# Kernel tuning notes

Measured on AMD Instinct MI355X. Metric: run time of the kernel, lower is better.

The kernel has to match this reference:

```python
import jax, jax.numpy as jnp
import numpy as np

# --- module hyperparameters (from init_kwargs) ---
IN_FEATURES = 256
TAU_MIN = 1.0
TAU_MAX = 20.0
K = 4
ALPHA = 1.0
NTAU = 100
SEQ_LEN = 2048
N_S = NTAU + 2 * K  # 108 taustars including k padding on both sides


def _laplace_constants():
    # c = (tau_max/tau_min)**(1/(ntau-1)) - 1
    c = (TAU_MAX / TAU_MIN) ** (1.0 / (NTAU - 1)) - 1.0
    tau_star = TAU_MIN * (1.0 + c) ** jnp.arange(-K, NTAU + K, dtype=jnp.float32)  # (N_S,)
    s = K / tau_star                      # (N_S,) decay rates
    e_s = jnp.exp(-s)                     # (N_S,)
    return s, e_s


def setup_inputs() -> dict:
    key = jax.random.key(0)
    inp = jax.random.normal(key, (SEQ_LEN, IN_FEATURES), dtype=jnp.float32)
    return {"inp": inp}


def reference(inp):
    """Laplace transform forward: diagonal linear recurrence over time.

    inp: (T, F) -> out: (T, N_S, F)
    t_n = e_alph_dur * t_{n-1} + decay * inp_n,  t_0 = 0
    """
    s, e_s = _laplace_constants()
    dur = TAU_MIN
    alpha = ALPHA
    e_alph_dur = e_s ** (dur * alpha)          # (N_S,)
    decay = (1.0 - e_alph_dur) / s             # (N_S,)

    # tIN[n, i, f] = decay[i] * inp[n, f]  -- matches matmul((N_S,1),(T,1,F))
    tIN = decay[None, :, None] * inp[:, None, :]   # (T, N_S, F)

    def step(t, x):
        t_new = e_alph_dur[:, None] * t + x
        return t_new, t_new

    t0 = jnp.zeros((N_S, inp.shape[1]), dtype=inp.dtype)
    _, out = jax.lax.scan(step, t0, tIN)       # (T, N_S, F)
    return out
```

## Files before the change

kernel.cpp:

```cpp
#include <hip/hip_runtime.h>


#define T_LEN 2048
#define F_DIM 256
#define NS    108
#define KPAD  4
#define CH    32
#define NB    (T_LEN / CH)

typedef float f32x4 __attribute__((ext_vector_type(4)));

__device__ __forceinline__ void laplace_consts(int i, float& s, float& e, float& decay) {
    const float c   = powf(20.0f, 1.0f / 99.0f) - 1.0f;
    const float tau = powf(1.0f + c, (float)(i - KPAD));
    s     = 4.0f / tau;
    e     = expf(-s);
    decay = (1.0f - e) / s;
}

__device__ __forceinline__ size_t ws_idx(int b, int i, int lane) {
    return (((size_t)b * NS + i) * 64 + lane) * 4;
}

__global__ __launch_bounds__(256) void laplace_local(
    const float* __restrict__ inp,
    float* __restrict__ ws)
{
    const int lane = threadIdx.x & 63;
    const int i    = blockIdx.y * 4 + (threadIdx.x >> 6);
    const int b    = blockIdx.x;

    float s, e, decay;
    laplace_consts(i, s, e, decay);

    const float* ip = inp + lane * 4;
    float t0 = 0.f, t1 = 0.f, t2 = 0.f, t3 = 0.f;

    const int n0 = b * CH;
    #pragma unroll 8
    for (int n = n0; n < n0 + CH; ++n) {
        f32x4 x = *(const f32x4*)(ip + (size_t)n * F_DIM);
        t0 = fmaf(e, t0, decay * x.x);
        t1 = fmaf(e, t1, decay * x.y);
        t2 = fmaf(e, t2, decay * x.z);
        t3 = fmaf(e, t3, decay * x.w);
    }
    f32x4 r; r.x = t0; r.y = t1; r.z = t2; r.w = t3;
    *(f32x4*)(ws + ws_idx(b, i, lane)) = r;
}

__global__ __launch_bounds__(256) void laplace_combine(
    float* __restrict__ ws)
{
    const int lane = threadIdx.x & 63;
    const int i    = blockIdx.x * 4 + (threadIdx.x >> 6);

    float s, e, decay;
    laplace_consts(i, s, e, decay);
    const float g = expf(-s * (float)CH);

    float S0 = 0.f, S1 = 0.f, S2 = 0.f, S3 = 0.f;
    #pragma unroll 8
    for (int b = 0; b < NB; ++b) {
        f32x4* p = (f32x4*)(ws + ws_idx(b, i, lane));
        f32x4 L = *p;
        f32x4 S; S.x = S0; S.y = S1; S.z = S2; S.w = S3;
        *p = S;
        S0 = fmaf(g, S0, L.x);
        S1 = fmaf(g, S1, L.y);
        S2 = fmaf(g, S2, L.z);
        S3 = fmaf(g, S3, L.w);
    }
}

__global__ __launch_bounds__(256) void laplace_main(
    const float* __restrict__ inp,
    const float* __restrict__ ws,
    float* __restrict__ out)
{
    const int lane = threadIdx.x & 63;
    const int f0   = lane * 4;
    const int i    = blockIdx.x * 4 + (threadIdx.x >> 6);
    const int b    = blockIdx.y;
    const int n0   = b * CH;

    float s, e, decay;
    laplace_consts(i, s, e, decay);

    f32x4 S = *(const f32x4*)(ws + ws_idx(b, i, lane));
    float t0 = S.x, t1 = S.y, t2 = S.z, t3 = S.w;

    const float* ip = inp + f0;
    float* op = out + (size_t)i * F_DIM + f0;

    #pragma unroll 8
    for (int n = n0; n < n0 + CH; ++n) {
        f32x4 x = *(const f32x4*)(ip + (size_t)n * F_DIM);
        t0 = fmaf(e, t0, decay * x.x);
        t1 = fmaf(e, t1, decay * x.y);
        t2 = fmaf(e, t2, decay * x.z);
        t3 = fmaf(e, t3, decay * x.w);
        f32x4 r; r.x = t0; r.y = t1; r.z = t2; r.w = t3;
        *(f32x4*)(op + (size_t)n * (NS * F_DIM)) = r;
    }
}

#define CHUNK_FB 64
#define WARM_FB  48
__global__ __launch_bounds__(256) void laplace_kernel_fb(
    const float* __restrict__ inp,
    float* __restrict__ out)
{
    const int tid  = threadIdx.x;
    const int lane = tid & 63;
    const int f0   = lane * 4;
    const int i    = blockIdx.y * 4 + (tid >> 6);
    const int n0   = blockIdx.x * CHUNK_FB;

    float s, e, decay;
    laplace_consts(i, s, e, decay);

    const float* ip = inp + f0;
    float t0 = 0.f, t1 = 0.f, t2 = 0.f, t3 = 0.f;

    int nstart = n0 - WARM_FB;
    if (nstart < 0) nstart = 0;
    #pragma unroll 4
    for (int n = nstart; n < n0; ++n) {
        f32x4 x = *(const f32x4*)(ip + (size_t)n * F_DIM);
        t0 = fmaf(e, t0, decay * x.x);
        t1 = fmaf(e, t1, decay * x.y);
        t2 = fmaf(e, t2, decay * x.z);
        t3 = fmaf(e, t3, decay * x.w);
    }
    float* op = out + (size_t)i * F_DIM + f0;
    #pragma unroll 4
    for (int n = n0; n < n0 + CHUNK_FB; ++n) {
        f32x4 x = *(const f32x4*)(ip + (size_t)n * F_DIM);
        t0 = fmaf(e, t0, decay * x.x);
        t1 = fmaf(e, t1, decay * x.y);
        t2 = fmaf(e, t2, decay * x.z);
        t3 = fmaf(e, t3, decay * x.w);
        f32x4 r; r.x = t0; r.y = t1; r.z = t2; r.w = t3;
        *(f32x4*)(op + (size_t)n * (NS * F_DIM)) = r;
    }
}

extern "C" void kernel_launch(void* const* d_in, const int* in_sizes, int n_in,
                              void* d_out, int out_size, void* d_ws, size_t ws_size,
                              hipStream_t stream) {
    const float* inp = (const float*)d_in[0];
    float* out = (float*)d_out;

    const size_t ws_need = (size_t)NB * NS * 64 * 4 * sizeof(float);

    if (d_ws != nullptr && ws_size >= ws_need) {
        float* ws = (float*)d_ws;
        laplace_local  <<<dim3(NB, NS / 4), 256, 0, stream>>>(inp, ws);
        laplace_combine<<<dim3(NS / 4),     256, 0, stream>>>(ws);
        laplace_main   <<<dim3(NS / 4, NB), 256, 0, stream>>>(inp, ws, out);
    } else {
        laplace_kernel_fb<<<dim3(T_LEN / CHUNK_FB, NS / 4), 256, 0, stream>>>(inp, out);
    }
}
```

Measured before the change: 235.1 us.

## Restructure main pass so each block handles all taustars for an 8-step time slice

The main pass is reorganised so each block owns an 8-timestep slice and all 108 taustar rows, with each wave holding 27 row states in registers. Every input row is loaded once and reused across all taustars, and each time step's writes cover a contiguous output row. The decay constants are computed once per block into shared memory. Because the slice starts mid-chunk, each block replays up to 24 steps from the chunk boundary, which adds redundant arithmetic and uses many registers, limiting occupancy to one block per CU.

```diff
diff --git a/kernel.cpp b/kernel.cpp
--- a/kernel.cpp
+++ b/kernel.cpp
@@ -7,6 +7,9 @@
 #define KPAD  4
 #define CH    32
 #define NB    (T_LEN / CH)
+#define CHC   8
+#define NBC   (T_LEN / CHC)
+#define NJ    27
 
 typedef float f32x4 __attribute__((ext_vector_type(4)));
 
@@ -73,35 +76,62 @@
     }
 }
 
-__global__ __launch_bounds__(256) void laplace_main(
+__global__ __launch_bounds__(256, 1) void laplace_slice(
     const float* __restrict__ inp,
     const float* __restrict__ ws,
     float* __restrict__ out)
 {
-    const int lane = threadIdx.x & 63;
+    __shared__ float sE[NS], sD[NS];
+    const int tid = threadIdx.x;
+    if (tid < NS) {
+        float s, e, d;
+        laplace_consts(tid, s, e, d);
+        sE[tid] = e; sD[tid] = d;
+    }
+    __syncthreads();
+
+    const int w    = tid >> 6;
+    const int lane = tid & 63;
     const int f0   = lane * 4;
-    const int i    = blockIdx.x * 4 + (threadIdx.x >> 6);
-    const int b    = blockIdx.y;
-    const int n0   = b * CH;
+    const int b2   = blockIdx.x;
+    const int n0   = b2 * CHC;
+    const int bb   = b2 >> 2;
+    const int base = bb * CH;
 
-    float s, e, decay;
-    laplace_consts(i, s, e, decay);
-
-    f32x4 S = *(const f32x4*)(ws + ws_idx(b, i, lane));
-    float t0 = S.x, t1 = S.y, t2 = S.z, t3 = S.w;
+    float eR[NJ], dR[NJ];
+    f32x4 st[NJ];
+    #pragma unroll
+    for (int j = 0; j < NJ; ++j) {
+        const int i = j * 4 + w;
+        eR[j] = sE[i];
+        dR[j] = sD[i];
+        st[j] = *(const f32x4*)(ws + ws_idx(bb, i, lane));
+    }
 
     const float* ip = inp + f0;
-    float* op = out + (size_t)i * F_DIM + f0;
 
-    #pragma unroll 8
-    for (int n = n0; n < n0 + CH; ++n) {
+    for (int n = base; n < n0; ++n) {
         f32x4 x = *(const f32x4*)(ip + (size_t)n * F_DIM);
-        t0 = fmaf(e, t0, decay * x.x);
-        t1 = fmaf(e, t1, decay * x.y);
-        t2 = fmaf(e, t2, decay * x.z);
-        t3 = fmaf(e, t3, decay * x.w);
-        f32x4 r; r.x = t0; r.y = t1; r.z = t2; r.w = t3;
-        *(f32x4*)(op + (size_t)n * (NS * F_DIM)) = r;
+        #pragma unroll
+        for (int j = 0; j < NJ; ++j) {
+            st[j].x = fmaf(eR[j], st[j].x, dR[j] * x.x);
+            st[j].y = fmaf(eR[j], st[j].y, dR[j] * x.y);
+            st[j].z = fmaf(eR[j], st[j].z, dR[j] * x.z);
+            st[j].w = fmaf(eR[j], st[j].w, dR[j] * x.w);
+        }
+    }
+
+    for (int n = n0; n < n0 + CHC; ++n) {
+        f32x4 x = *(const f32x4*)(ip + (size_t)n * F_DIM);
+        float* op = out + (size_t)n * (NS * F_DIM) + f0;
+        #pragma unroll
+        for (int j = 0; j < NJ; ++j) {
+            st[j].x = fmaf(eR[j], st[j].x, dR[j] * x.x);
+            st[j].y = fmaf(eR[j], st[j].y, dR[j] * x.y);
+            st[j].z = fmaf(eR[j], st[j].z, dR[j] * x.z);
+            st[j].w = fmaf(eR[j], st[j].w, dR[j] * x.w);
+            *(f32x4*)(op + (size_t)(j * 4 + w) * F_DIM) = st[j];
+        }
     }
 }
 
@@ -158,7 +188,7 @@
         float* ws = (float*)d_ws;
         laplace_local  <<<dim3(NB, NS / 4), 256, 0, stream>>>(inp, ws);
         laplace_combine<<<dim3(NS / 4),     256, 0, stream>>>(ws);
-        laplace_main   <<<dim3(NS / 4, NB), 256, 0, stream>>>(inp, ws, out);
+        laplace_slice  <<<dim3(NBC),        256, 0, stream>>>(inp, ws, out);
     } else {
         laplace_kernel_fb<<<dim3(T_LEN / CHUNK_FB, NS / 4), 256, 0, stream>>>(inp, out);
     }
```

Measured after the change: 249.4 us. 1.06x slower.
